# Performance work log

Measured on AMD Instinct MI355X. Metric: run time of the kernel, lower is better.

## Reference

```python
import jax, jax.numpy as jnp
import numpy as np

B, NUM, LQ, LP, H = 8, 4, 128, 512, 512


def setup_inputs() -> dict:
    key = jax.random.key(0)
    k1, k2, k3 = jax.random.split(key, 3)
    return {
        "encode_input1": jax.random.normal(k1, (B, NUM, LQ, H), jnp.float32),
        "encode_input2": jax.random.normal(k2, (B, NUM, LP, H), jnp.float32),
        "input1_mask": jnp.ones((B, NUM, LQ), jnp.int32),
        "input2_mask": jnp.ones((B, NUM, LP), jnp.int32),
        "w": jax.random.normal(k3, (3 * H,), jnp.float32) * (1.0 / np.sqrt(3 * H)),
    }


def reference(encode_input1, encode_input2, input1_mask, input2_mask, w):
    Bb, num_q, Lq, Hh = encode_input1.shape
    _, num_p, Lp, _ = encode_input2.shape
    # num_q == num_p path of the original module
    E_q = encode_input1.reshape(-1, Lq, Hh)            # [BM, Lq, H]
    E_p = encode_input2.reshape(-1, Lp, Hh)            # [BM, Lp, H]
    m_q = input1_mask.reshape(-1, Lq)
    m_p = input2_mask.reshape(-1, Lp)
    # Linear([E_q, E_p, E_q*E_p]) -> scalar decomposes into three terms;
    # avoids materializing the O(Lp*Lq*3H) broadcast-concat tensor.
    w_q, w_p, w_m = w[:Hh], w[Hh:2 * Hh], w[2 * Hh:]
    U = ((E_p @ w_p)[:, :, None]
         + (E_q @ w_q)[:, None, :]
         + jnp.einsum('bph,h,bqh->bpq', E_p, w_m, E_q))   # [BM, Lp, Lq]
    mask = (m_p[:, :, None] * m_q[:, None, :]).astype(bool)
    Um = jnp.where(mask, U, jnp.finfo(U.dtype).min)
    A_p = jnp.where(mask, jax.nn.softmax(Um, axis=2), 0.0)   # row softmax over Lq
    B_p = jnp.where(mask, jax.nn.softmax(Um, axis=1), 0.0)   # col softmax over Lp
    A1 = A_p @ E_q                                   # [BM, Lp, H]
    B1 = jnp.einsum('bpq,bph->bqh', B_p, E_p)        # [BM, Lq, H]
    A2 = A_p @ B1                                    # [BM, Lp, H]
    B2 = jnp.einsum('bpq,bph->bqh', B_p, A1)         # [BM, Lq, H]
    shp_p = (Bb, num_p, Lp, Hh)
    shp_q = (Bb, num_p, Lq, Hh)
    E_p4 = E_p.reshape(shp_p); E_q4 = E_q.reshape(shp_q)
    A1 = A1.reshape(shp_p); A2 = A2.reshape(shp_p)
    B1 = B1.reshape(shp_q); B2 = B2.reshape(shp_q)
    G_q_p = jnp.concatenate([E_p4, A1, A2, E_p4 * A1, E_p4 * A2], axis=-1)
    G_p_q = jnp.concatenate([E_q4, B1, B2, E_q4 * B1, E_q4 * B2], axis=-1)
    G_p_q = G_p_q * input1_mask[..., None].astype(G_p_q.dtype)
    G_q_p = G_q_p * input2_mask[..., None].astype(G_q_p.dtype)
    return (G_p_q, G_q_p)
```

## Files before the change

### kernel.cpp

```cpp
#include <hip/hip_runtime.h>
#include <hip/hip_bf16.h>

#define BBATCH 32
#define LQ 128
#define LP 512
#define HDIM 512
#define GDIM 2560
#define NEG_MAX (-3.402823466e38f)

typedef __attribute__((ext_vector_type(8))) short short8;
typedef __attribute__((ext_vector_type(4))) float f32x4;
typedef __attribute__((ext_vector_type(4))) unsigned short ushort4v;

__device__ inline unsigned short f2bf(float f) {
  union { float f; unsigned int u; } v; v.f = f;
  unsigned int r = v.u + 0x7FFFu + ((v.u >> 16) & 1u);
  return (unsigned short)(r >> 16);
}

__device__ inline void stage128x64(const unsigned short* __restrict__ src, int ld,
                                   int row0, int k0, unsigned short* lds, int t) {
#pragma unroll
  for (int i = 0; i < 4; i++) {
    int o = (t + i * 256) * 16;
    int row = o >> 7, col = (o & 127) >> 1;
    int swz = o ^ ((row & 7) << 4);
    *(short8*)((char*)lds + swz) = *(const short8*)(src + (long)(row0 + row) * ld + k0 + col);
  }
}
__device__ inline void stage64x64_f32(const float* __restrict__ src, int ld,
                                      int row0, int k0, unsigned short* lds, int t) {
#pragma unroll
  for (int i = 0; i < 2; i++) {
    int o = (t + i * 256) * 16;
    int row = o >> 7, col = (o & 127) >> 1;
    int swz = o ^ ((row & 7) << 4);
    const float* p = src + (long)(row0 + row) * ld + k0 + col;
    float4 a = *(const float4*)p;
    float4 b2 = *(const float4*)(p + 4);
    short8 v = {(short)f2bf(a.x), (short)f2bf(a.y), (short)f2bf(a.z), (short)f2bf(a.w),
                (short)f2bf(b2.x), (short)f2bf(b2.y), (short)f2bf(b2.z), (short)f2bf(b2.w)};
    *(short8*)((char*)lds + swz) = v;
  }
}
__device__ inline short8 fragld(const unsigned short* lds, int row, int ks, int fq) {
  return *(const short8*)((const char*)lds + (((row << 7) + ks * 64 + fq * 16) ^ ((row & 7) << 4)));
}

__global__ __launch_bounds__(256) void prep_kernel(
    const float* __restrict__ Ep, const float* __restrict__ Eq,
    const float* __restrict__ w,
    unsigned short* __restrict__ EpT, unsigned short* __restrict__ EqT,
    unsigned short* __restrict__ Eqw,
    float* __restrict__ epv, float* __restrict__ eqv) {
  const int b = blockIdx.y;
  const int bx = blockIdx.x;
  const bool isP = bx < 8;
  const int R = isP ? LP : LQ;
  const int p0 = (isP ? bx : bx - 8) * 64;
  const float* src = isP ? Ep + (long)b * LP * HDIM : Eq + (long)b * LQ * HDIM;
  const float* wb_base = isP ? w + HDIM : w;
  unsigned short* dT = isP ? EpT + (long)b * HDIM * LP : EqT + (long)b * HDIM * LQ;
  unsigned short* dW = isP ? nullptr : Eqw + (long)b * LQ * HDIM;
  float* bias = (isP ? epv + b * LP : eqv + b * LQ) + p0;
  __shared__ float T[64][65];
  const int t = threadIdx.x, c4 = (t & 15) * 4, r = t >> 4;
  float dot[4] = {0.f, 0.f, 0.f, 0.f};
  for (int h0 = 0; h0 < HDIM; h0 += 64) {
    float4 wb = *(const float4*)(wb_base + h0 + c4);
    float4 wm4 = {0, 0, 0, 0};
    if (!isP) wm4 = *(const float4*)(w + 2 * HDIM + h0 + c4);
    __syncthreads();
#pragma unroll
    for (int i = 0; i < 4; i++) {
      int row = r + 16 * i;
      float4 v = *(const float4*)(src + (long)(p0 + row) * HDIM + h0 + c4);
      T[row][c4] = v.x; T[row][c4 + 1] = v.y; T[row][c4 + 2] = v.z; T[row][c4 + 3] = v.w;
      if (!isP) {
        ushort4v ow = {f2bf(v.x * wm4.x), f2bf(v.y * wm4.y), f2bf(v.z * wm4.z), f2bf(v.w * wm4.w)};
        *(ushort4v*)(dW + (long)(p0 + row) * HDIM + h0 + c4) = ow;
      }
      dot[i] += v.x * wb.x + v.y * wb.y + v.z * wb.z + v.w * wb.w;
    }
    __syncthreads();
#pragma unroll
    for (int i = 0; i < 4; i++) {
      int hh = r + 16 * i;
      ushort4v o = {f2bf(T[c4][hh]), f2bf(T[c4 + 1][hh]), f2bf(T[c4 + 2][hh]), f2bf(T[c4 + 3][hh])};
      *(ushort4v*)(dT + (long)(h0 + hh) * R + p0 + c4) = o;
    }
  }
#pragma unroll
  for (int i = 0; i < 4; i++) {
#pragma unroll
    for (int s = 1; s < 16; s <<= 1) dot[i] += __shfl_xor(dot[i], s);
  }
  if ((t & 15) == 0) {
#pragma unroll
    for (int i = 0; i < 4; i++) bias[r + 16 * i] = dot[i];
  }
}

__global__ __launch_bounds__(256) void u_gemm(
    const float* __restrict__ EpF, const unsigned short* __restrict__ Bb,
    const float* __restrict__ epv, const float* __restrict__ eqv,
    const int* __restrict__ maskM, const int* __restrict__ maskN,
    float* __restrict__ UmT, unsigned short* __restrict__ Apb) {
  const int hw = blockIdx.x;
  const int xcd = hw & 7, s_ = hw >> 3;
  const int b = xcd * 4 + (s_ >> 3);
  const int m0 = (s_ & 7) * 64;
  const float* A = EpF + (long)b * LP * HDIM;
  const unsigned short* B = Bb + (long)b * LQ * HDIM;
  __shared__ unsigned short As[4096];
  __shared__ unsigned short Bs[8192];
  __shared__ float smax[2][64], ssum[2][64];
  const int t = threadIdx.x, lane = t & 63, wid = t >> 6;
  const int wm = wid >> 1, wn = wid & 1;
  const int wr = wm * 32, wc = wn * 64;
  const int fr = lane & 15, fq = lane >> 4;
  f32x4 acc[2][4] = {};
  for (int k0 = 0; k0 < HDIM; k0 += 64) {
    stage64x64_f32(A, HDIM, m0, k0, As, t);
    stage128x64(B, HDIM, 0, k0, Bs, t);
    __syncthreads();
#pragma unroll
    for (int ks = 0; ks < 2; ks++) {
      short8 af[2], bfv[4];
#pragma unroll
      for (int i = 0; i < 2; i++) af[i] = fragld(As, wr + i * 16 + fr, ks, fq);
#pragma unroll
      for (int j = 0; j < 4; j++) bfv[j] = fragld(Bs, wc + j * 16 + fr, ks, fq);
#pragma unroll
      for (int i = 0; i < 2; i++)
#pragma unroll
        for (int j = 0; j < 4; j++)
          acc[i][j] = __builtin_amdgcn_mfma_f32_16x16x32_bf16(af[i], bfv[j], acc[i][j], 0, 0, 0);
    }
    __syncthreads();
  }
  const float* ep_b = epv + (long)b * LP;
  const float* eq_b = eqv + (long)b * LQ;
  const int* mM = maskM + (long)b * LP;
  const int* mN = maskN + (long)b * LQ;
  float* UmTB = UmT + (long)b * LQ * LP;
  unsigned short* ApB = Apb + (long)b * LP * LQ;
  float eqc[4]; int mnc[4];
#pragma unroll
  for (int j = 0; j < 4; j++) {
    int col = wc + j * 16 + fr;
    eqc[j] = eq_b[col]; mnc[j] = mN[col];
  }
  float epr[2][4]; int mmr[2][4];
#pragma unroll
  for (int i = 0; i < 2; i++)
#pragma unroll
    for (int r = 0; r < 4; r++) {
      int row = m0 + wr + i * 16 + fq * 4 + r;
      epr[i][r] = ep_b[row]; mmr[i][r] = mM[row];
    }
#pragma unroll
  for (int i = 0; i < 2; i++)
#pragma unroll
    for (int j = 0; j < 4; j++) {
      float4 tv;
#pragma unroll
      for (int r = 0; r < 4; r++) {
        float a = acc[i][j][r];
        bool ok = mmr[i][r] && mnc[j];
        ((float*)&tv)[r] = ok ? a + epr[i][r] : NEG_MAX;
        acc[i][j][r] = ok ? a + eqc[j] : NEG_MAX;
      }
      int col = wc + j * 16 + fr;
      *(float4*)(UmTB + (long)col * LP + m0 + wr + i * 16 + fq * 4) = tv;
    }
  float mx[2][4];
#pragma unroll
  for (int i = 0; i < 2; i++)
#pragma unroll
    for (int r = 0; r < 4; r++) {
      float m = fmaxf(fmaxf(acc[i][0][r], acc[i][1][r]), fmaxf(acc[i][2][r], acc[i][3][r]));
#pragma unroll
      for (int s = 1; s < 16; s <<= 1) m = fmaxf(m, __shfl_xor(m, s));
      mx[i][r] = m;
      if (fr == 0) smax[wn][wr + i * 16 + fq * 4 + r] = m;
    }
  __syncthreads();
#pragma unroll
  for (int i = 0; i < 2; i++)
#pragma unroll
    for (int r = 0; r < 4; r++) {
      int rl = wr + i * 16 + fq * 4 + r;
      mx[i][r] = fmaxf(smax[0][rl], smax[1][rl]);
    }
#pragma unroll
  for (int i = 0; i < 2; i++)
#pragma unroll
    for (int r = 0; r < 4; r++) {
      float s = 0.f;
#pragma unroll
      for (int j = 0; j < 4; j++) {
        float e = __expf(acc[i][j][r] - mx[i][r]);
        acc[i][j][r] = e; s += e;
      }
#pragma unroll
      for (int sh = 1; sh < 16; sh <<= 1) s += __shfl_xor(s, sh);
      if (fr == 0) ssum[wn][wr + i * 16 + fq * 4 + r] = s;
    }
  __syncthreads();
#pragma unroll
  for (int i = 0; i < 2; i++)
#pragma unroll
    for (int r = 0; r < 4; r++) {
      int rl = wr + i * 16 + fq * 4 + r;
      float S = ssum[0][rl] + ssum[1][rl];
      float inv = S > 0.f ? 1.f / S : 0.f;
      int row = m0 + rl;
#pragma unroll
      for (int j = 0; j < 4; j++) {
        int col = wc + j * 16 + fr;
        bool ok = mmr[i][r] && mnc[j];
        ApB[(long)row * LQ + col] = ok ? f2bf(acc[i][j][r] * inv) : 0;
      }
    }
}

__global__ __launch_bounds__(256) void colsoftmaxT_kernel(
    const float* __restrict__ UmT, unsigned short* __restrict__ BpT,
    const int* __restrict__ mp, const int* __restrict__ mq) {
  int wid = blockIdx.x * 4 + (threadIdx.x >> 6);
  int lane = threadIdx.x & 63;
  int b = wid >> 7;
  const float* row = UmT + (long)wid * LP;
  float v[8];
  float m = NEG_MAX;
#pragma unroll
  for (int i = 0; i < 8; i++) { v[i] = row[lane + 64 * i]; m = fmaxf(m, v[i]); }
#pragma unroll
  for (int off = 32; off; off >>= 1) m = fmaxf(m, __shfl_xor(m, off));
  float e[8];
  float s = 0.f;
#pragma unroll
  for (int i = 0; i < 8; i++) { e[i] = __expf(v[i] - m); s += e[i]; }
#pragma unroll
  for (int off = 32; off; off >>= 1) s += __shfl_xor(s, off);
  float inv = s > 0.f ? 1.f / s : 0.f;
  int mqv = mq[wid];
#pragma unroll
  for (int i = 0; i < 8; i++) {
    int p = lane + 64 * i;
    bool ok = mqv && mp[b * LP + p];
    BpT[(long)wid * LP + p] = ok ? f2bf(e[i] * inv) : 0;
  }
}

template <int PHASE>
__global__ __launch_bounds__(256) void gemm_phase(
    const unsigned short* __restrict__ Apb, const unsigned short* __restrict__ BpT,
    const unsigned short* __restrict__ BA, const unsigned short* __restrict__ BB,
    const float* __restrict__ EpF, const float* __restrict__ EqF,
    const int* __restrict__ mp, const int* __restrict__ mq,
    float* __restrict__ out_gqp, float* __restrict__ out_gpq,
    unsigned short* __restrict__ A1T, unsigned short* __restrict__ B1T) {
  const int hw = blockIdx.x;
  const int xcd = hw & 7, s_ = hw >> 3;
  const int b = xcd * 4 + (s_ / 20);
  const int bx = s_ % 20;
  __shared__ __align__(16) char smem[32768];
  unsigned short* As = (unsigned short*)smem;
  unsigned short* Bs = (unsigned short*)(smem + 16384);
  float (*Cs)[132] = (float(*)[132])smem;
  const int t = threadIdx.x, lane = t & 63, wid = t >> 6;
  const int wr = (wid >> 1) * 64, wc = (wid & 1) * 64;
  const int fr = lane & 15, fq = lane >> 4;
  const unsigned short* A; const unsigned short* Bop;
  int K, M, m0, n0;
  float* outBase; const float* Eb; const int* mb;
  unsigned short* Tout;
  if (bx < 4) {
    A = BpT + (long)b * LQ * LP; K = LP; M = LQ; m0 = 0; n0 = bx * 128;
    Bop = BB + (long)b * HDIM * LP;
    outBase = out_gpq + (long)b * LQ * GDIM;
    Eb = EqF + (long)b * LQ * HDIM; mb = mq + (long)b * LQ;
    Tout = (PHASE == 1) ? B1T + (long)b * HDIM * LQ : nullptr;
  } else {
    int idx = bx - 4; m0 = (idx >> 2) * 128; n0 = (idx & 3) * 128;
    A = Apb + (long)b * LP * LQ; K = LQ; M = LP;
    Bop = BA + (long)b * HDIM * LQ;
    outBase = out_gqp + (long)b * LP * GDIM;
    Eb = EpF + (long)b * LP * HDIM; mb = mp + (long)b * LP;
    Tout = (PHASE == 1) ? A1T + (long)b * HDIM * LP : nullptr;
  }
  f32x4 acc[4][4] = {};
  for (int k0 = 0; k0 < K; k0 += 64) {
    stage128x64(A, K, m0, k0, As, t);
    stage128x64(Bop, K, n0, k0, Bs, t);
    __syncthreads();
#pragma unroll
    for (int ks = 0; ks < 2; ks++) {
      short8 af[4], bfv[4];
#pragma unroll
      for (int i = 0; i < 4; i++) {
        af[i] = fragld(As, wr + i * 16 + fr, ks, fq);
        bfv[i] = fragld(Bs, wc + i * 16 + fr, ks, fq);
      }
#pragma unroll
      for (int i = 0; i < 4; i++)
#pragma unroll
        for (int j = 0; j < 4; j++)
          acc[i][j] = __builtin_amdgcn_mfma_f32_16x16x32_bf16(af[i], bfv[j], acc[i][j], 0, 0, 0);
    }
    __syncthreads();
  }
  if (PHASE == 1) {
#pragma unroll
    for (int i = 0; i < 4; i++)
#pragma unroll
      for (int j = 0; j < 4; j++) {
        int col = n0 + wc + j * 16 + fr;
        int row0 = m0 + wr + i * 16 + fq * 4;
        ushort4v o = {f2bf(acc[i][j][0]), f2bf(acc[i][j][1]),
                      f2bf(acc[i][j][2]), f2bf(acc[i][j][3])};
        *(ushort4v*)(Tout + (long)col * M + row0) = o;
      }
  }
  const int band = wid >> 1;
#pragma unroll
  for (int i = 0; i < 4; i++) {
    __syncthreads();
#pragma unroll
    for (int j = 0; j < 4; j++) {
#pragma unroll
      for (int r = 0; r < 4; r++)
        Cs[band * 16 + fq * 4 + r][wc + j * 16 + fr] = acc[i][j][r];
    }
    __syncthreads();
#pragma unroll
    for (int k = 0; k < 4; k++) {
      int slot = t + k * 256;
      int row_l = slot >> 5;
      int c4 = (slot & 31) * 4;
      int bnd = row_l >> 4;
      int r_g = m0 + bnd * 64 + i * 16 + (row_l & 15);
      float mm = (float)mb[r_g];
      f32x4 v = *(f32x4*)&Cs[row_l][c4];
      f32x4 e = *(const f32x4*)(Eb + (long)r_g * HDIM + n0 + c4);
      float* orow = outBase + (long)r_g * GDIM + n0 + c4;
      f32x4 vm = v * mm;
      f32x4 evm = e * vm;
      if (PHASE == 1) {
        __builtin_nontemporal_store(e * mm, (f32x4*)(orow));
        __builtin_nontemporal_store(vm, (f32x4*)(orow + HDIM));
        __builtin_nontemporal_store(evm, (f32x4*)(orow + 3 * HDIM));
      } else {
        __builtin_nontemporal_store(vm, (f32x4*)(orow + 2 * HDIM));
        __builtin_nontemporal_store(evm, (f32x4*)(orow + 4 * HDIM));
      }
    }
  }
}

extern "C" void kernel_launch(void* const* d_in, const int* in_sizes, int n_in,
                              void* d_out, int out_size, void* d_ws, size_t ws_size,
                              hipStream_t stream) {
  const float* Eq = (const float*)d_in[0];
  const float* Ep = (const float*)d_in[1];
  const int* mq = (const int*)d_in[2];
  const int* mp = (const int*)d_in[3];
  const float* w = (const float*)d_in[4];
  float* out = (float*)d_out;
  float* out_gpq = out;
  float* out_gqp = out + (long)BBATCH * LQ * GDIM;

  unsigned short* EpT = (unsigned short*)d_ws;
  unsigned short* EqT = EpT + 32L * 512 * 512;
  unsigned short* Eqw = EqT + 32L * 512 * 128;
  unsigned short* Apb = Eqw + 32L * 128 * 512;
  unsigned short* BpT = Apb + 32L * 512 * 128;
  unsigned short* B1T = BpT + 32L * 128 * 512;
  unsigned short* A1T = B1T + 32L * 512 * 128;
  float* UmT = (float*)(A1T + 32L * 512 * 512);
  float* epb = UmT + 32L * 128 * 512;
  float* eqb2 = epb + 32L * 512;

  prep_kernel<<<dim3(10, BBATCH), 256, 0, stream>>>(
      Ep, Eq, w, EpT, EqT, Eqw, epb, eqb2);

  u_gemm<<<dim3(256), 256, 0, stream>>>(
      Ep, Eqw, epb, eqb2, mp, mq, UmT, Apb);

  colsoftmaxT_kernel<<<BBATCH * LQ / 4, 256, 0, stream>>>(UmT, BpT, mp, mq);

  gemm_phase<1><<<dim3(640), 256, 0, stream>>>(
      Apb, BpT, EqT, EpT, Ep, Eq, mp, mq, out_gqp, out_gpq, A1T, B1T);

  gemm_phase<2><<<dim3(640), 256, 0, stream>>>(
      Apb, BpT, B1T, A1T, Ep, Eq, mp, mq, out_gqp, out_gpq, nullptr, nullptr);
}
```

Measured before the change: 107.2 us.

## Fuse column softmax into the phase GEMMs' A-operand staging

Removes the separate column-softmax kernel and its bf16 BpT buffer. In both GEMM phases, the blocks that handle the Lq-side product now compute per-row max and inverse sum from fp32 UmT themselves. They then apply exp and normalisation while staging the A tile into LDS. This saves one launch and one write-plus-read of the probability matrix. In exchange, every one of those blocks recomputes the row statistics in each phase, reads the A operand in fp32 instead of bf16, and evaluates exp per element, which lengthens the already longest K=512 blocks. The p-side mask is no longer applied to the column probabilities.

Measured after the change: 155.5 us. +45.1%, slower.

```diff
diff --git a/kernel.cpp b/kernel.cpp
--- a/kernel.cpp
+++ b/kernel.cpp
@@ -40,6 +40,25 @@
     float4 b2 = *(const float4*)(p + 4);
     short8 v = {(short)f2bf(a.x), (short)f2bf(a.y), (short)f2bf(a.z), (short)f2bf(a.w),
                 (short)f2bf(b2.x), (short)f2bf(b2.y), (short)f2bf(b2.z), (short)f2bf(b2.w)};
+    *(short8*)((char*)lds + swz) = v;
+  }
+}
+__device__ inline void stageU(const float* __restrict__ Ub, int k0,
+                              const float* __restrict__ Mv, const float* __restrict__ Iv,
+                              unsigned short* lds, int t) {
+#pragma unroll
+  for (int i = 0; i < 4; i++) {
+    int o = (t + i * 256) * 16;
+    int row = o >> 7, col = (o & 127) >> 1;
+    int swz = o ^ ((row & 7) << 4);
+    const float* p = Ub + (long)row * LP + k0 + col;
+    float4 a = *(const float4*)p;
+    float4 b2 = *(const float4*)(p + 4);
+    float M = Mv[row], I = Iv[row];
+    short8 v = {(short)f2bf(__expf(a.x - M) * I), (short)f2bf(__expf(a.y - M) * I),
+                (short)f2bf(__expf(a.z - M) * I), (short)f2bf(__expf(a.w - M) * I),
+                (short)f2bf(__expf(b2.x - M) * I), (short)f2bf(__expf(b2.y - M) * I),
+                (short)f2bf(__expf(b2.z - M) * I), (short)f2bf(__expf(b2.w - M) * I)};
     *(short8*)((char*)lds + swz) = v;
   }
 }
@@ -225,38 +244,9 @@
     }
 }
 
-__global__ __launch_bounds__(256) void colsoftmaxT_kernel(
-    const float* __restrict__ UmT, unsigned short* __restrict__ BpT,
-    const int* __restrict__ mp, const int* __restrict__ mq) {
-  int wid = blockIdx.x * 4 + (threadIdx.x >> 6);
-  int lane = threadIdx.x & 63;
-  int b = wid >> 7;
-  const float* row = UmT + (long)wid * LP;
-  float v[8];
-  float m = NEG_MAX;
-#pragma unroll
-  for (int i = 0; i < 8; i++) { v[i] = row[lane + 64 * i]; m = fmaxf(m, v[i]); }
-#pragma unroll
-  for (int off = 32; off; off >>= 1) m = fmaxf(m, __shfl_xor(m, off));
-  float e[8];
-  float s = 0.f;
-#pragma unroll
-  for (int i = 0; i < 8; i++) { e[i] = __expf(v[i] - m); s += e[i]; }
-#pragma unroll
-  for (int off = 32; off; off >>= 1) s += __shfl_xor(s, off);
-  float inv = s > 0.f ? 1.f / s : 0.f;
-  int mqv = mq[wid];
-#pragma unroll
-  for (int i = 0; i < 8; i++) {
-    int p = lane + 64 * i;
-    bool ok = mqv && mp[b * LP + p];
-    BpT[(long)wid * LP + p] = ok ? f2bf(e[i] * inv) : 0;
-  }
-}
-
 template <int PHASE>
 __global__ __launch_bounds__(256) void gemm_phase(
-    const unsigned short* __restrict__ Apb, const unsigned short* __restrict__ BpT,
+    const unsigned short* __restrict__ Apb, const float* __restrict__ UmT,
     const unsigned short* __restrict__ BA, const unsigned short* __restrict__ BB,
     const float* __restrict__ EpF, const float* __restrict__ EqF,
     const int* __restrict__ mp, const int* __restrict__ mq,
@@ -266,19 +256,22 @@
   const int xcd = hw & 7, s_ = hw >> 3;
   const int b = xcd * 4 + (s_ / 20);
   const int bx = s_ % 20;
-  __shared__ __align__(16) char smem[32768];
+  __shared__ __align__(16) char smem[33792];
   unsigned short* As = (unsigned short*)smem;
   unsigned short* Bs = (unsigned short*)(smem + 16384);
   float (*Cs)[132] = (float(*)[132])smem;
+  float* Mv = (float*)(smem + 32768);
+  float* Iv = (float*)(smem + 32768 + 512);
   const int t = threadIdx.x, lane = t & 63, wid = t >> 6;
   const int wr = (wid >> 1) * 64, wc = (wid & 1) * 64;
   const int fr = lane & 15, fq = lane >> 4;
-  const unsigned short* A; const unsigned short* Bop;
+  const unsigned short* A = nullptr; const unsigned short* Bop;
+  const float* Ub = nullptr;
   int K, M, m0, n0;
   float* outBase; const float* Eb; const int* mb;
   unsigned short* Tout;
   if (bx < 4) {
-    A = BpT + (long)b * LQ * LP; K = LP; M = LQ; m0 = 0; n0 = bx * 128;
+    Ub = UmT + (long)b * LQ * LP; K = LP; M = LQ; m0 = 0; n0 = bx * 128;
     Bop = BB + (long)b * HDIM * LP;
     outBase = out_gpq + (long)b * LQ * GDIM;
     Eb = EqF + (long)b * LQ * HDIM; mb = mq + (long)b * LQ;
@@ -291,9 +284,33 @@
     Eb = EpF + (long)b * LP * HDIM; mb = mp + (long)b * LP;
     Tout = (PHASE == 1) ? A1T + (long)b * HDIM * LP : nullptr;
   }
+  if (bx < 4) {
+    const int* mqb = mq + (long)b * LQ;
+    const int wv = wid;
+    for (int rr = 0; rr < 32; rr++) {
+      int q = wv * 32 + rr;
+      const float* row = Ub + (long)q * LP;
+      float v[8]; float m = NEG_MAX;
+#pragma unroll
+      for (int i = 0; i < 8; i++) { v[i] = row[lane + 64 * i]; m = fmaxf(m, v[i]); }
+#pragma unroll
+      for (int off = 32; off; off >>= 1) m = fmaxf(m, __shfl_xor(m, off));
+      float s = 0.f;
+#pragma unroll
+      for (int i = 0; i < 8; i++) s += __expf(v[i] - m);
+#pragma unroll
+      for (int off = 32; off; off >>= 1) s += __shfl_xor(s, off);
+      if (lane == 0) {
+        Mv[q] = m;
+        Iv[q] = (mqb[q] && m > -1e37f && s > 0.f) ? 1.f / s : 0.f;
+      }
+    }
+    __syncthreads();
+  }
   f32x4 acc[4][4] = {};
   for (int k0 = 0; k0 < K; k0 += 64) {
-    stage128x64(A, K, m0, k0, As, t);
+    if (bx < 4) stageU(Ub, k0, Mv, Iv, As, t);
+    else stage128x64(A, K, m0, k0, As, t);
     stage128x64(Bop, K, n0, k0, Bs, t);
     __syncthreads();
 #pragma unroll
@@ -376,8 +393,7 @@
   unsigned short* EqT = EpT + 32L * 512 * 512;
   unsigned short* Eqw = EqT + 32L * 512 * 128;
   unsigned short* Apb = Eqw + 32L * 128 * 512;
-  unsigned short* BpT = Apb + 32L * 512 * 128;
-  unsigned short* B1T = BpT + 32L * 128 * 512;
+  unsigned short* B1T = Apb + 32L * 512 * 128;
   unsigned short* A1T = B1T + 32L * 512 * 128;
   float* UmT = (float*)(A1T + 32L * 512 * 512);
   float* epb = UmT + 32L * 128 * 512;
@@ -389,11 +405,9 @@
   u_gemm<<<dim3(256), 256, 0, stream>>>(
       Ep, Eqw, epb, eqb2, mp, mq, UmT, Apb);
 
-  colsoftmaxT_kernel<<<BBATCH * LQ / 4, 256, 0, stream>>>(UmT, BpT, mp, mq);
-
   gemm_phase<1><<<dim3(640), 256, 0, stream>>>(
-      Apb, BpT, EqT, EpT, Ep, Eq, mp, mq, out_gqp, out_gpq, A1T, B1T);
+      Apb, UmT, EqT, EpT, Ep, Eq, mp, mq, out_gqp, out_gpq, A1T, B1T);
 
   gemm_phase<2><<<dim3(640), 256, 0, stream>>>(
-      Apb, BpT, B1T, A1T, Ep, Eq, mp, mq, out_gqp, out_gpq, nullptr, nullptr);
-}
+      Apb, UmT, B1T, A1T, Ep, Eq, mp, mq, out_gqp, out_gpq, nullptr, nullptr);
+}
```
